# Optimization experiments

Measured on AMD Instinct MI355X. Metric: run time of the kernel, lower is better.

The kernel has to match this reference:

```python
import jax, jax.numpy as jnp
import numpy as np

M = 150        # AR2 tail-fit window
LAM = 1e-3     # ridge regularizer in the 2x2 solve
CLIP_K = 4.0   # soft clip multiplier
H = 96         # forecast horizon (base_model.H)


def setup_inputs() -> dict:
    key = jax.random.key(0)
    k1, k2 = jax.random.split(key)
    x = jax.random.normal(k1, (32, 512, 2048), dtype=jnp.float32)
    W = jax.random.normal(k2, (2048, 96), dtype=jnp.float32) * 0.02
    return {"x": x, "W": W}


def _ar2_forecast(x):
    # x: (B, C, L); closed-form AR2 fit on last M samples, vectorized over (B, C)
    y = x[..., -M:]                     # (B, C, M)
    Y = y[..., 2:]                      # targets
    p1 = y[..., 1:-1]
    p2 = y[..., :-2]
    s = lambda a, b: jnp.sum(a * b, axis=-1)
    A11 = s(p1, p1) + LAM
    A22 = s(p2, p2) + LAM
    A12 = s(p1, p2)
    b1 = s(p1, Y)
    b2 = s(p2, Y)
    det = A11 * A22 - A12 * A12
    a1 = (b1 * A22 - b2 * A12) / det    # (B, C)
    a2 = (A11 * b2 - A12 * b1) / det

    def step(carry, _):
        y1, y2 = carry
        yn = a1 * y1 + a2 * y2
        return (yn, y1), yn

    _, out = jax.lax.scan(step, (x[..., -1], x[..., -2]), None, length=H)
    return jnp.moveaxis(out, 0, -1)     # (B, C, H)


def reference(x, W):
    # AR2 part is computed on detached history in the original (numpy round-trip)
    Yb = jax.lax.stop_gradient(_ar2_forecast(x))
    d_hat = jnp.einsum('bcl,lh->bch', x, W)          # base model: per-channel linear head
    y_hat = Yb + d_hat
    last = x[..., -1:]                               # (B, C, 1), broadcasts over H
    hstd = jnp.maximum(jnp.std(x, axis=-1, ddof=1, keepdims=True), 1e-6)  # torch unbiased std
    return jnp.clip(y_hat, last - CLIP_K * hstd, last + CLIP_K * hstd)
```

## Files before the change

### kernel.cpp

```cpp
#include <hip/hip_runtime.h>
#include <math.h>

constexpr int L     = 2048;
constexpr int NH    = 96;
constexpr int MLEN  = 150;
constexpr int NAR   = 148;
constexpr float LAM    = 0.001f;
constexpr float CLIP_K = 4.0f;

constexpr int TM     = 32;
constexpr int KM     = 64;
constexpr int MSTEPS = L / KM;

typedef __attribute__((ext_vector_type(8))) short short8;
typedef __attribute__((ext_vector_type(4))) float floatx4;

__device__ inline short f2bf(float f) {
    union { float f; unsigned u; } v; v.f = f;
    unsigned r = v.u + 0x7FFFu + ((v.u >> 16) & 1u);
    return (short)(r >> 16);
}

__global__ __launch_bounds__(256) void wt_kernel(
    const float* __restrict__ W, short* __restrict__ Wt)
{
    int idx = blockIdx.x * 256 + threadIdx.x;
    int n = idx >> 11;
    int k = idx & 2047;
    Wt[idx] = f2bf(W[k * NH + n]);
}

__global__ __launch_bounds__(256) void gemm_ar2_kernel(
    const float* __restrict__ x, const short* __restrict__ Wt,
    float* __restrict__ out)
{
    __shared__ float As[2][TM * KM];
    __shared__ short Bs[2][NH * KM];
    __shared__ float Ys[TM][NH + 1];
    __shared__ float los[TM], his[TM];

    const int t    = threadIdx.x;
    const int lane = t & 63;
    const int wv   = t >> 6;
    const int h    = wv >> 1;
    const int g    = wv & 1;
    const int m    = lane & 15;
    const int quad = lane >> 4;
    const int row0 = blockIdx.x * TM;
    const int r    = h * 16 + m;

    const int cA0 = wv * 128 + lane, cA1 = cA0 + 64;
    const int rA0 = cA0 >> 4, chA0 = cA0 & 15;
    const int rA1 = cA1 >> 4, chA1 = cA1 & 15;
    const float* pa0 = x + (size_t)(row0 + rA0) * L
                         + ((chA0 >> 3) * 32 + ((chA0 & 7) ^ (rA0 & 7)) * 4);
    const float* pa1 = x + (size_t)(row0 + rA1) * L
                         + ((chA1 >> 3) * 32 + ((chA1 & 7) ^ (rA1 & 7)) * 4);

    const int cB0 = wv * 192 + lane, cB1 = cB0 + 64, cB2 = cB0 + 128;
    const short* pb0 = Wt + (size_t)(cB0 >> 3) * L + (((cB0 & 7) ^ ((cB0 >> 3) & 7)) * 8);
    const short* pb1 = Wt + (size_t)(cB1 >> 3) * L + (((cB1 & 7) ^ ((cB1 >> 3) & 7)) * 8);
    const short* pb2 = Wt + (size_t)(cB2 >> 3) * L + (((cB2 & 7) ^ ((cB2 >> 3) & 7)) * 8);

    floatx4 acc[3];
    #pragma unroll
    for (int jj = 0; jj < 3; ++jj) acc[jj] = floatx4{0.f, 0.f, 0.f, 0.f};
    float sum = 0.f, sumsq = 0.f;

    const int pA0 = (2 * quad)     ^ (m & 7);
    const int pA1 = (2 * quad + 1) ^ (m & 7);

    auto stage = [&](int buf, int k0) {
        __builtin_amdgcn_global_load_lds(
            (const __attribute__((address_space(1))) unsigned int*)(pa0 + k0),
            (__attribute__((address_space(3))) unsigned int*)&As[buf][wv * 512], 16, 0, 0);
        __builtin_amdgcn_global_load_lds(
            (const __attribute__((address_space(1))) unsigned int*)(pa1 + k0),
            (__attribute__((address_space(3))) unsigned int*)&As[buf][wv * 512 + 256], 16, 0, 0);
        __builtin_amdgcn_global_load_lds(
            (const __attribute__((address_space(1))) unsigned int*)(pb0 + k0),
            (__attribute__((address_space(3))) unsigned int*)&Bs[buf][wv * 1536], 16, 0, 0);
        __builtin_amdgcn_global_load_lds(
            (const __attribute__((address_space(1))) unsigned int*)(pb1 + k0),
            (__attribute__((address_space(3))) unsigned int*)&Bs[buf][wv * 1536 + 512], 16, 0, 0);
        __builtin_amdgcn_global_load_lds(
            (const __attribute__((address_space(1))) unsigned int*)(pb2 + k0),
            (__attribute__((address_space(3))) unsigned int*)&Bs[buf][wv * 1536 + 1024], 16, 0, 0);
    };

    stage(0, 0);

    for (int s = 0; s < MSTEPS; ++s) {
        const int cur = s & 1;
        __syncthreads();
        if (s + 1 < MSTEPS) stage(cur ^ 1, (s + 1) * KM);

        #pragma unroll
        for (int ss = 0; ss < 2; ++ss) {
            float4 f0 = *(const float4*)&As[cur][r * KM + ss * 32 + pA0 * 4];
            float4 f1 = *(const float4*)&As[cur][r * KM + ss * 32 + pA1 * 4];

            if (g == 0) {
                sum  += ((f0.x + f0.y) + (f0.z + f0.w))
                      + ((f1.x + f1.y) + (f1.z + f1.w));
                sumsq = fmaf(f0.x, f0.x, sumsq); sumsq = fmaf(f0.y, f0.y, sumsq);
                sumsq = fmaf(f0.z, f0.z, sumsq); sumsq = fmaf(f0.w, f0.w, sumsq);
                sumsq = fmaf(f1.x, f1.x, sumsq); sumsq = fmaf(f1.y, f1.y, sumsq);
                sumsq = fmaf(f1.z, f1.z, sumsq); sumsq = fmaf(f1.w, f1.w, sumsq);
            }

            short8 af;
            af[0] = f2bf(f0.x); af[1] = f2bf(f0.y); af[2] = f2bf(f0.z); af[3] = f2bf(f0.w);
            af[4] = f2bf(f1.x); af[5] = f2bf(f1.y); af[6] = f2bf(f1.z); af[7] = f2bf(f1.w);

            const int bch = ((ss * 4 + quad) ^ (m & 7)) * 8;
            #pragma unroll
            for (int jj = 0; jj < 3; ++jj) {
                short8 bf = *(const short8*)&Bs[cur][(g * 48 + jj * 16 + m) * KM + bch];
                acc[jj] = __builtin_amdgcn_mfma_f32_16x16x32_bf16(af, bf, acc[jj], 0, 0, 0);
            }
        }
    }

    if (g == 0) {
        sum   += __shfl_xor(sum,   16); sum   += __shfl_xor(sum,   32);
        sumsq += __shfl_xor(sumsq, 16); sumsq += __shfl_xor(sumsq, 32);

        const float* ytail = x + (size_t)(row0 + r) * L + (L - MLEN);
        float A11 = 0.f, A22 = 0.f, A12 = 0.f, b1 = 0.f, b2 = 0.f;
        for (int i = quad; i < NAR; i += 4) {
            float p2v = ytail[i];
            float p1v = ytail[i + 1];
            float Yv  = ytail[i + 2];
            A11 = fmaf(p1v, p1v, A11);
            A22 = fmaf(p2v, p2v, A22);
            A12 = fmaf(p1v, p2v, A12);
            b1  = fmaf(p1v, Yv,  b1);
            b2  = fmaf(p2v, Yv,  b2);
        }
        A11 += __shfl_xor(A11, 16); A11 += __shfl_xor(A11, 32);
        A22 += __shfl_xor(A22, 16); A22 += __shfl_xor(A22, 32);
        A12 += __shfl_xor(A12, 16); A12 += __shfl_xor(A12, 32);
        b1  += __shfl_xor(b1,  16); b1  += __shfl_xor(b1,  32);
        b2  += __shfl_xor(b2,  16); b2  += __shfl_xor(b2,  32);

        if (quad == 0) {
            A11 += LAM; A22 += LAM;
            float det = A11 * A22 - A12 * A12;
            float a1c = (b1 * A22 - b2 * A12) / det;
            float a2c = (A11 * b2 - A12 * b1) / det;

            float last = ytail[MLEN - 1];
            float y1 = last;
            float y2 = ytail[MLEN - 2];
            for (int n = 0; n < NH; ++n) {
                float yn = a1c * y1 + a2c * y2;
                Ys[r][n] = yn;
                y2 = y1; y1 = yn;
            }
            float var  = (sumsq - sum * sum * (1.0f / L)) * (1.0f / (L - 1));
            float hstd = fmaxf(sqrtf(fmaxf(var, 0.f)), 1e-6f);
            los[r] = last - CLIP_K * hstd;
            his[r] = last + CLIP_K * hstd;
        }
    }
    __syncthreads();

    #pragma unroll
    for (int reg = 0; reg < 4; ++reg) {
        int rl = h * 16 + quad * 4 + reg;
        float lo = los[rl], hi = his[rl];
        #pragma unroll
        for (int jj = 0; jj < 3; ++jj) {
            int c = (3 * g + jj) * 16 + m;
            float v = acc[jj][reg] + Ys[rl][c];
            v = fminf(fmaxf(v, lo), hi);
            out[(size_t)(row0 + rl) * NH + c] = v;
        }
    }
}

extern "C" void kernel_launch(void* const* d_in, const int* in_sizes, int n_in,
                              void* d_out, int out_size, void* d_ws, size_t ws_size,
                              hipStream_t stream) {
    const float* x = (const float*)d_in[0];
    const float* W = (const float*)d_in[1];
    float* out = (float*)d_out;
    short* Wt  = (short*)d_ws;

    wt_kernel<<<dim3((NH * L) / 256), dim3(256), 0, stream>>>(W, Wt);

    const int rows = 32 * 512;
    gemm_ar2_kernel<<<dim3(rows / TM), dim3(256), 0, stream>>>(x, Wt, out);
}
```

Measured before the change: 207.2 us.

## Halve row tile and split K across wave pairs with LDS reduction

The row tile drops from 32 to 16 rows per block, which doubles the grid from 512 to 1024 blocks. The four waves are regrouped so that two wave pairs each take half of every 64-wide K chunk for the same 16 rows. Their partial MFMA accumulators and statistics are then reduced through shared memory, reusing the B buffer as scratch. Launch bounds ask for 4 blocks per CU, aiming at more occupancy and better CU fill. The cost is that each block reloads the full W tile for only half as many rows, which doubles W traffic per output, plus an extra reduction barrier.

Result: no change. 209.9 us (+1.3%).

```diff
diff --git a/kernel.cpp b/kernel.cpp
--- a/kernel.cpp
+++ b/kernel.cpp
@@ -8,7 +8,7 @@
 constexpr float LAM    = 0.001f;
 constexpr float CLIP_K = 4.0f;
 
-constexpr int TM     = 32;
+constexpr int TM     = 16;
 constexpr int KM     = 64;
 constexpr int MSTEPS = L / KM;
 
@@ -30,7 +30,7 @@
     Wt[idx] = f2bf(W[k * NH + n]);
 }
 
-__global__ __launch_bounds__(256) void gemm_ar2_kernel(
+__global__ __launch_bounds__(256, 4) void gemm_ar2_kernel(
     const float* __restrict__ x, const short* __restrict__ Wt,
     float* __restrict__ out)
 {
@@ -38,24 +38,20 @@
     __shared__ short Bs[2][NH * KM];
     __shared__ float Ys[TM][NH + 1];
     __shared__ float los[TM], his[TM];
+    __shared__ float s2[TM], q2[TM];
 
     const int t    = threadIdx.x;
     const int lane = t & 63;
     const int wv   = t >> 6;
-    const int h    = wv >> 1;
     const int g    = wv & 1;
+    const int e    = wv >> 1;
     const int m    = lane & 15;
     const int quad = lane >> 4;
     const int row0 = blockIdx.x * TM;
-    const int r    = h * 16 + m;
-
-    const int cA0 = wv * 128 + lane, cA1 = cA0 + 64;
-    const int rA0 = cA0 >> 4, chA0 = cA0 & 15;
-    const int rA1 = cA1 >> 4, chA1 = cA1 & 15;
-    const float* pa0 = x + (size_t)(row0 + rA0) * L
-                         + ((chA0 >> 3) * 32 + ((chA0 & 7) ^ (rA0 & 7)) * 4);
-    const float* pa1 = x + (size_t)(row0 + rA1) * L
-                         + ((chA1 >> 3) * 32 + ((chA1 & 7) ^ (rA1 & 7)) * 4);
+
+    const int rA = t >> 4, chA = t & 15;
+    const float* pa = x + (size_t)(row0 + rA) * L
+                        + ((chA >> 3) * 32 + ((chA & 7) ^ (rA & 7)) * 4);
 
     const int cB0 = wv * 192 + lane, cB1 = cB0 + 64, cB2 = cB0 + 128;
     const short* pb0 = Wt + (size_t)(cB0 >> 3) * L + (((cB0 & 7) ^ ((cB0 >> 3) & 7)) * 8);
@@ -72,11 +68,8 @@
 
     auto stage = [&](int buf, int k0) {
         __builtin_amdgcn_global_load_lds(
-            (const __attribute__((address_space(1))) unsigned int*)(pa0 + k0),
-            (__attribute__((address_space(3))) unsigned int*)&As[buf][wv * 512], 16, 0, 0);
-        __builtin_amdgcn_global_load_lds(
-            (const __attribute__((address_space(1))) unsigned int*)(pa1 + k0),
-            (__attribute__((address_space(3))) unsigned int*)&As[buf][wv * 512 + 256], 16, 0, 0);
+            (const __attribute__((address_space(1))) unsigned int*)(pa + k0),
+            (__attribute__((address_space(3))) unsigned int*)&As[buf][wv * 256], 16, 0, 0);
         __builtin_amdgcn_global_load_lds(
             (const __attribute__((address_space(1))) unsigned int*)(pb0 + k0),
             (__attribute__((address_space(3))) unsigned int*)&Bs[buf][wv * 1536], 16, 0, 0);
@@ -95,87 +88,112 @@
         __syncthreads();
         if (s + 1 < MSTEPS) stage(cur ^ 1, (s + 1) * KM);
 
-        #pragma unroll
-        for (int ss = 0; ss < 2; ++ss) {
-            float4 f0 = *(const float4*)&As[cur][r * KM + ss * 32 + pA0 * 4];
-            float4 f1 = *(const float4*)&As[cur][r * KM + ss * 32 + pA1 * 4];
-
-            if (g == 0) {
-                sum  += ((f0.x + f0.y) + (f0.z + f0.w))
-                      + ((f1.x + f1.y) + (f1.z + f1.w));
-                sumsq = fmaf(f0.x, f0.x, sumsq); sumsq = fmaf(f0.y, f0.y, sumsq);
-                sumsq = fmaf(f0.z, f0.z, sumsq); sumsq = fmaf(f0.w, f0.w, sumsq);
-                sumsq = fmaf(f1.x, f1.x, sumsq); sumsq = fmaf(f1.y, f1.y, sumsq);
-                sumsq = fmaf(f1.z, f1.z, sumsq); sumsq = fmaf(f1.w, f1.w, sumsq);
+        float4 f0 = *(const float4*)&As[cur][m * KM + e * 32 + pA0 * 4];
+        float4 f1 = *(const float4*)&As[cur][m * KM + e * 32 + pA1 * 4];
+
+        if (g == 0) {
+            sum  += ((f0.x + f0.y) + (f0.z + f0.w))
+                  + ((f1.x + f1.y) + (f1.z + f1.w));
+            sumsq = fmaf(f0.x, f0.x, sumsq); sumsq = fmaf(f0.y, f0.y, sumsq);
+            sumsq = fmaf(f0.z, f0.z, sumsq); sumsq = fmaf(f0.w, f0.w, sumsq);
+            sumsq = fmaf(f1.x, f1.x, sumsq); sumsq = fmaf(f1.y, f1.y, sumsq);
+            sumsq = fmaf(f1.z, f1.z, sumsq); sumsq = fmaf(f1.w, f1.w, sumsq);
+        }
+
+        short8 af;
+        af[0] = f2bf(f0.x); af[1] = f2bf(f0.y); af[2] = f2bf(f0.z); af[3] = f2bf(f0.w);
+        af[4] = f2bf(f1.x); af[5] = f2bf(f1.y); af[6] = f2bf(f1.z); af[7] = f2bf(f1.w);
+
+        const int bch = ((e * 4 + quad) ^ (m & 7)) * 8;
+        #pragma unroll
+        for (int jj = 0; jj < 3; ++jj) {
+            short8 bf = *(const short8*)&Bs[cur][(g * 48 + jj * 16 + m) * KM + bch];
+            acc[jj] = __builtin_amdgcn_mfma_f32_16x16x32_bf16(af, bf, acc[jj], 0, 0, 0);
+        }
+    }
+
+    float* ar = (float*)&Bs[0][0];
+    if (e == 1) {
+        #pragma unroll
+        for (int jj = 0; jj < 3; ++jj)
+            #pragma unroll
+            for (int reg = 0; reg < 4; ++reg)
+                ar[(g * 64 + lane) * 12 + jj * 4 + reg] = acc[jj][reg];
+        if (g == 0) {
+            float su = sum, sq = sumsq;
+            su += __shfl_xor(su, 16); su += __shfl_xor(su, 32);
+            sq += __shfl_xor(sq, 16); sq += __shfl_xor(sq, 32);
+            if (quad == 0) { s2[m] = su; q2[m] = sq; }
+        }
+    }
+    __syncthreads();
+
+    if (e == 0) {
+        #pragma unroll
+        for (int jj = 0; jj < 3; ++jj)
+            #pragma unroll
+            for (int reg = 0; reg < 4; ++reg)
+                acc[jj][reg] += ar[(g * 64 + lane) * 12 + jj * 4 + reg];
+
+        if (g == 0) {
+            sum   += __shfl_xor(sum,   16); sum   += __shfl_xor(sum,   32);
+            sumsq += __shfl_xor(sumsq, 16); sumsq += __shfl_xor(sumsq, 32);
+
+            const float* ytail = x + (size_t)(row0 + m) * L + (L - MLEN);
+            float A11 = 0.f, A22 = 0.f, A12 = 0.f, b1 = 0.f, b2 = 0.f;
+            for (int i = quad; i < NAR; i += 4) {
+                float p2v = ytail[i];
+                float p1v = ytail[i + 1];
+                float Yv  = ytail[i + 2];
+                A11 = fmaf(p1v, p1v, A11);
+                A22 = fmaf(p2v, p2v, A22);
+                A12 = fmaf(p1v, p2v, A12);
+                b1  = fmaf(p1v, Yv,  b1);
+                b2  = fmaf(p2v, Yv,  b2);
             }
-
-            short8 af;
-            af[0] = f2bf(f0.x); af[1] = f2bf(f0.y); af[2] = f2bf(f0.z); af[3] = f2bf(f0.w);
-            af[4] = f2bf(f1.x); af[5] = f2bf(f1.y); af[6] = f2bf(f1.z); af[7] = f2bf(f1.w);
-
-            const int bch = ((ss * 4 + quad) ^ (m & 7)) * 8;
+            A11 += __shfl_xor(A11, 16); A11 += __shfl_xor(A11, 32);
+            A22 += __shfl_xor(A22, 16); A22 += __shfl_xor(A22, 32);
+            A12 += __shfl_xor(A12, 16); A12 += __shfl_xor(A12, 32);
+            b1  += __shfl_xor(b1,  16); b1  += __shfl_xor(b1,  32);
+            b2  += __shfl_xor(b2,  16); b2  += __shfl_xor(b2,  32);
+
+            if (quad == 0) {
+                sum   += s2[m];
+                sumsq += q2[m];
+                A11 += LAM; A22 += LAM;
+                float det = A11 * A22 - A12 * A12;
+                float a1c = (b1 * A22 - b2 * A12) / det;
+                float a2c = (A11 * b2 - A12 * b1) / det;
+
+                float last = ytail[MLEN - 1];
+                float y1 = last;
+                float y2 = ytail[MLEN - 2];
+                for (int n = 0; n < NH; ++n) {
+                    float yn = a1c * y1 + a2c * y2;
+                    Ys[m][n] = yn;
+                    y2 = y1; y1 = yn;
+                }
+                float var  = (sumsq - sum * sum * (1.0f / L)) * (1.0f / (L - 1));
+                float hstd = fmaxf(sqrtf(fmaxf(var, 0.f)), 1e-6f);
+                los[m] = last - CLIP_K * hstd;
+                his[m] = last + CLIP_K * hstd;
+            }
+        }
+    }
+    __syncthreads();
+
+    if (e == 0) {
+        #pragma unroll
+        for (int reg = 0; reg < 4; ++reg) {
+            int rl = quad * 4 + reg;
+            float lo = los[rl], hi = his[rl];
             #pragma unroll
             for (int jj = 0; jj < 3; ++jj) {
-                short8 bf = *(const short8*)&Bs[cur][(g * 48 + jj * 16 + m) * KM + bch];
-                acc[jj] = __builtin_amdgcn_mfma_f32_16x16x32_bf16(af, bf, acc[jj], 0, 0, 0);
+                int c = (3 * g + jj) * 16 + m;
+                float v = acc[jj][reg] + Ys[rl][c];
+                v = fminf(fmaxf(v, lo), hi);
+                out[(size_t)(row0 + rl) * NH + c] = v;
             }
-        }
-    }
-
-    if (g == 0) {
-        sum   += __shfl_xor(sum,   16); sum   += __shfl_xor(sum,   32);
-        sumsq += __shfl_xor(sumsq, 16); sumsq += __shfl_xor(sumsq, 32);
-
-        const float* ytail = x + (size_t)(row0 + r) * L + (L - MLEN);
-        float A11 = 0.f, A22 = 0.f, A12 = 0.f, b1 = 0.f, b2 = 0.f;
-        for (int i = quad; i < NAR; i += 4) {
-            float p2v = ytail[i];
-            float p1v = ytail[i + 1];
-            float Yv  = ytail[i + 2];
-            A11 = fmaf(p1v, p1v, A11);
-            A22 = fmaf(p2v, p2v, A22);
-            A12 = fmaf(p1v, p2v, A12);
-            b1  = fmaf(p1v, Yv,  b1);
-            b2  = fmaf(p2v, Yv,  b2);
-        }
-        A11 += __shfl_xor(A11, 16); A11 += __shfl_xor(A11, 32);
-        A22 += __shfl_xor(A22, 16); A22 += __shfl_xor(A22, 32);
-        A12 += __shfl_xor(A12, 16); A12 += __shfl_xor(A12, 32);
-        b1  += __shfl_xor(b1,  16); b1  += __shfl_xor(b1,  32);
-        b2  += __shfl_xor(b2,  16); b2  += __shfl_xor(b2,  32);
-
-        if (quad == 0) {
-            A11 += LAM; A22 += LAM;
-            float det = A11 * A22 - A12 * A12;
-            float a1c = (b1 * A22 - b2 * A12) / det;
-            float a2c = (A11 * b2 - A12 * b1) / det;
-
-            float last = ytail[MLEN - 1];
-            float y1 = last;
-            float y2 = ytail[MLEN - 2];
-            for (int n = 0; n < NH; ++n) {
-                float yn = a1c * y1 + a2c * y2;
-                Ys[r][n] = yn;
-                y2 = y1; y1 = yn;
-            }
-            float var  = (sumsq - sum * sum * (1.0f / L)) * (1.0f / (L - 1));
-            float hstd = fmaxf(sqrtf(fmaxf(var, 0.f)), 1e-6f);
-            los[r] = last - CLIP_K * hstd;
-            his[r] = last + CLIP_K * hstd;
-        }
-    }
-    __syncthreads();
-
-    #pragma unroll
-    for (int reg = 0; reg < 4; ++reg) {
-        int rl = h * 16 + quad * 4 + reg;
-        float lo = los[rl], hi = his[rl];
-        #pragma unroll
-        for (int jj = 0; jj < 3; ++jj) {
-            int c = (3 * g + jj) * 16 + m;
-            float v = acc[jj][reg] + Ys[rl][c];
-            v = fminf(fmaxf(v, lo), hi);
-            out[(size_t)(row0 + rl) * NH + c] = v;
         }
     }
 }
```
